# Kernel optimization log

Hardware: AMD Instinct MI355X
Metric: run time of the kernel (lower is better)

## Reference

```python
import jax, jax.numpy as jnp
import numpy as np

N, M, A, F = 8000, 12, 64, 64
EPS = 1e-5


def setup_inputs() -> dict:
    key = jax.random.key(0)
    ks = jax.random.split(key, 8)
    rn = lambda k, s, sc=0.05: jax.random.normal(k, s, jnp.float32) * sc
    return {
        "atom_in_fea": rn(ks[0], (N, A), 1.0),
        "nbr_fea": rn(ks[1], (N, M, F), 1.0),
        "nbr_fea_idx": jax.random.randint(ks[2], (N, M), 0, N),
        # fc_full: in = 2A+F, out = 2A (stored as (in, out))
        "W_full": rn(ks[3], (2 * A + F, 2 * A)), "b_full": jnp.zeros((2 * A,), jnp.float32),
        "bn1_gamma": jnp.ones((2 * A,), jnp.float32), "bn1_beta": jnp.zeros((2 * A,), jnp.float32),
        # fc_edge: in = 2A+F, out = 2F
        "W_edge": rn(ks[4], (2 * A + F, 2 * F)), "b_edge": jnp.zeros((2 * F,), jnp.float32),
        "bne_gamma": jnp.ones((2 * F,), jnp.float32), "bne_beta": jnp.zeros((2 * F,), jnp.float32),
        # fc_3body: in = 3A+2F, out = 2A
        "W_3body": rn(ks[5], (3 * A + 2 * F, 2 * A)), "b_3body": jnp.zeros((2 * A,), jnp.float32),
        "bn3_gamma": jnp.ones((2 * A,), jnp.float32), "bn3_beta": jnp.zeros((2 * A,), jnp.float32),
        # bn2 over atom_fea_len
        "bn2_gamma": jnp.ones((A,), jnp.float32), "bn2_beta": jnp.zeros((A,), jnp.float32),
    }


def _bn(x, gamma, beta):
    # training-mode BatchNorm1d: batch stats over all but the last (channel) axis, biased var
    axes = tuple(range(x.ndim - 1))
    mean = jnp.mean(x, axes, keepdims=True)
    var = jnp.mean(jnp.square(x - mean), axes, keepdims=True)
    return (x - mean) * jax.lax.rsqrt(var + EPS) * gamma + beta


def _gate(z, axis):
    filt, core = jnp.split(z, 2, axis=-1)
    return jnp.sum(jax.nn.sigmoid(filt) * jax.nn.softplus(core), axis=axis)


def reference(atom_in_fea, nbr_fea, nbr_fea_idx,
              W_full, b_full, bn1_gamma, bn1_beta,
              W_edge, b_edge, bne_gamma, bne_beta,
              W_3body, b_3body, bn3_gamma, bn3_beta,
              bn2_gamma, bn2_beta):
    a_len = atom_in_fea.shape[1]
    f_len = nbr_fea.shape[2]
    atom_nbr = atom_in_fea[nbr_fea_idx]                       # (N, M, A) gather
    total = jnp.concatenate([
        jnp.broadcast_to(atom_in_fea[:, None, :], atom_nbr.shape),
        atom_nbr, nbr_fea], axis=-1)                           # (N, M, 2A+F)

    # 2-body gated update
    g = _bn(total @ W_full + b_full, bn1_gamma, bn1_beta)      # (N, M, 2A)
    two_body = _gate(g, axis=1)                                # (N, A)

    # explicit edge update
    e = _bn(total @ W_edge + b_edge, bne_gamma, bne_beta)      # (N, M, 2F)
    ef, ec = jnp.split(e, 2, axis=-1)
    nbr_out_fea = nbr_fea + jax.nn.sigmoid(ef) * jax.nn.softplus(ec)

    # 3-body term: Linear over concat([x_i, x_j, x_l, e_ij, e_il]) decomposed so we never
    # materialize the (N, M, M, 3A+2F) concat; only the (N, M, M, 2A) projection exists.
    Wa, Wj, Wl, Wij, Wil = jnp.split(
        W_3body, [a_len, 2 * a_len, 3 * a_len, 3 * a_len + f_len], axis=0)
    p_i = atom_in_fea @ Wa                                     # (N, 2A)
    p_j = atom_nbr @ Wj + nbr_fea @ Wij                        # (N, M, 2A) j/ij part
    p_l = atom_nbr @ Wl + nbr_fea @ Wil                        # (N, M, 2A) l/il part
    z = p_i[:, None, None, :] + p_j[:, :, None, :] + p_l[:, None, :, :] + b_3body
    z = _bn(z, bn3_gamma, bn3_beta)                            # (N, M, M, 2A)
    three_body = _gate(z, axis=(1, 2))                         # (N, A)

    total_summed = _bn(two_body + three_body, bn2_gamma, bn2_beta)
    atom_out_fea = jax.nn.softplus(atom_in_fea + total_summed)
    return (atom_out_fea, nbr_out_fea)
```

## Files before the change

kernel.cpp:

```cpp
#include <hip/hip_runtime.h>

typedef unsigned short u16;
typedef unsigned int u32;
typedef __attribute__((ext_vector_type(8))) short short8;
typedef __attribute__((ext_vector_type(4))) float f32x4;

#define NATOMS 8000
#define MNBR 12
#define EPSV 1e-5f
#define AB 4
#define ROWS 48
#define NBLK 2000
#define K2REC 1664

#define STG_B 12672
__device__ __forceinline__ int stg_idx(int row, int col) {
  return (row >> 2) * 528 + (row & 3) * 128 + col;
}

#define XB_OFF 0
#define WTA_OFF 1024000
#define WTE_OFF 1122304
#define WAT_OFF 1187840
#define SSUM_OFF 1220608
#define PARAMS_OFF 1227776
#define TBUF_OFF 1230848
#define WS_NEED 3278848

#define SS_BN1S 0
#define SS_BN1S2 128
#define SS_BNES 256
#define SS_BNES2 384
#define SS_U2 512
#define SS_V2 640
#define SS_A 768
#define SS_A2 896
#define SS_UB 1024
#define SS_VB 1152
#define SS_AU 1280
#define SS_AV 1408
#define SS_UV 1536

__device__ __forceinline__ u16 f2bf(float f) {
  u32 u = __float_as_uint(f);
  u += 0x7FFFu + ((u >> 16) & 1u);
  return (u16)(u >> 16);
}
__device__ __forceinline__ float bf2f(u16 h) { return __uint_as_float(((u32)h) << 16); }

__device__ __forceinline__ float sigf(float x) {
  return __builtin_amdgcn_rcpf(1.f + __expf(-x));
}
__device__ __forceinline__ float spf(float x) {
  return fmaxf(x, 0.f) + __logf(1.f + __expf(-fabsf(x)));
}

__device__ __forceinline__ void mfma16(f32x4 &acc, short8 a, short8 b) {
  asm volatile("v_mfma_f32_16x16x32_bf16 %0, %1, %2, %0" : "+v"(acc) : "v"(a), "v"(b));
}
__device__ __forceinline__ void accfence(f32x4 &a) {
  asm volatile("s_nop 7\ns_nop 7\ns_nop 7" : "+v"(a));
}
__device__ __forceinline__ void initfence(f32x4 &a) {
  asm volatile("s_nop 1" : "+v"(a));
}

__device__ __forceinline__ void stage_row16(short* lds, int row, int c16, const float* __restrict__ src) {
  const float4* s4 = reinterpret_cast<const float4*>(src);
  float4 q0 = s4[0], q1 = s4[1], q2 = s4[2], q3 = s4[3];
  short8 lo, hi;
  lo[0]=(short)f2bf(q0.x); lo[1]=(short)f2bf(q0.y); lo[2]=(short)f2bf(q0.z); lo[3]=(short)f2bf(q0.w);
  lo[4]=(short)f2bf(q1.x); lo[5]=(short)f2bf(q1.y); lo[6]=(short)f2bf(q1.z); lo[7]=(short)f2bf(q1.w);
  hi[0]=(short)f2bf(q2.x); hi[1]=(short)f2bf(q2.y); hi[2]=(short)f2bf(q2.z); hi[3]=(short)f2bf(q2.w);
  hi[4]=(short)f2bf(q3.x); hi[5]=(short)f2bf(q3.y); hi[6]=(short)f2bf(q3.z); hi[7]=(short)f2bf(q3.w);
  int base = row * 128 + c16 * 2;
  int sw = (row & 7) << 4;
  *reinterpret_cast<short8*>(reinterpret_cast<char*>(lds) + (base ^ sw)) = lo;
  *reinterpret_cast<short8*>(reinterpret_cast<char*>(lds) + ((base + 16) ^ sw)) = hi;
}

__device__ __forceinline__ void stage_xj(const u16* __restrict__ XB, const int* __restrict__ nidx,
                                         int eb, int ab, char* xjT, int t) {
  for (int s = t; s < 512; s += 256) {
    int r = s >> 3, j = s & 7;
    uint4 val = make_uint4(0u, 0u, 0u, 0u);
    if (r < 48) {
      int idx = nidx[eb + r];
      val = *reinterpret_cast<const uint4*>(XB + (size_t)idx * 64 + j * 8);
    } else if (r < 52) {
      val = *reinterpret_cast<const uint4*>(XB + (size_t)(ab + r - 48) * 64 + j * 8);
    }
    int off = (r * 128 + j * 16) ^ ((r & 7) << 4);
    *reinterpret_cast<uint4*>(xjT + off) = val;
  }
}

__device__ __forceinline__ short8 lds_afrag(const short* lds, int row, int kbyte) {
  int off = (row * 128 + kbyte) ^ ((row & 7) << 4);
  return *reinterpret_cast<const short8*>(reinterpret_cast<const char*>(lds) + off);
}

template <int RT>
__device__ __forceinline__ void mfma_dual(const short* xjT, const short* nbrT,
                                          const u16* __restrict__ WTA, const u16* __restrict__ WTE,
                                          int baseA, int baseE, int w, int l,
                                          f32x4 (&acc)[RT][2]) {
  short8 ba[2][2], be[2][2];
#pragma unroll
  for (int p = 0; p < 2; ++p) {
    int colg = ((w + p * 4) << 4) + (l & 15);
#pragma unroll
    for (int kc = 0; kc < 2; ++kc) {
      ba[p][kc] = *reinterpret_cast<const short8*>(WTA + (size_t)(baseA + colg) * 64 + kc * 32 + ((l >> 4) << 3));
      be[p][kc] = *reinterpret_cast<const short8*>(WTE + (size_t)(baseE + colg) * 64 + kc * 32 + ((l >> 4) << 3));
    }
  }
#pragma unroll
  for (int rt = 0; rt < RT; ++rt)
#pragma unroll
    for (int p = 0; p < 2; ++p) { acc[rt][p] = f32x4{0.f, 0.f, 0.f, 0.f}; initfence(acc[rt][p]); }
#pragma unroll
  for (int rt = 0; rt < RT; ++rt) {
    int arow = rt * 16 + (l & 15);
    short8 x0 = lds_afrag(xjT, arow, (l >> 4) << 4);
    short8 x1 = lds_afrag(xjT, arow, 64 + ((l >> 4) << 4));
    short8 n0 = lds_afrag(nbrT, arow, (l >> 4) << 4);
    short8 n1 = lds_afrag(nbrT, arow, 64 + ((l >> 4) << 4));
#pragma unroll
    for (int p = 0; p < 2; ++p) {
      mfma16(acc[rt][p], x0, ba[p][0]);
      mfma16(acc[rt][p], x1, ba[p][1]);
      mfma16(acc[rt][p], n0, be[p][0]);
      mfma16(acc[rt][p], n1, be[p][1]);
    }
  }
#pragma unroll
  for (int rt = 0; rt < RT; ++rt)
#pragma unroll
    for (int p = 0; p < 2; ++p) accfence(acc[rt][p]);
}

__device__ __forceinline__ void mfma_own(const short* xjT, const u16* __restrict__ WTA,
                                         int baseO, int w, int l, float* ownv) {
  short8 bo[2][2];
#pragma unroll
  for (int p = 0; p < 2; ++p) {
    int colg = ((w + p * 4) << 4) + (l & 15);
#pragma unroll
    for (int kc = 0; kc < 2; ++kc)
      bo[p][kc] = *reinterpret_cast<const short8*>(WTA + (size_t)(baseO + colg) * 64 + kc * 32 + ((l >> 4) << 3));
  }
  int arow = 48 + (l & 15);
  short8 x0 = lds_afrag(xjT, arow, (l >> 4) << 4);
  short8 x1 = lds_afrag(xjT, arow, 64 + ((l >> 4) << 4));
  f32x4 acc[2];
#pragma unroll
  for (int p = 0; p < 2; ++p) {
    acc[p] = f32x4{0.f, 0.f, 0.f, 0.f};
    initfence(acc[p]);
    mfma16(acc[p], x0, bo[p][0]);
    mfma16(acc[p], x1, bo[p][1]);
  }
#pragma unroll
  for (int p = 0; p < 2; ++p) accfence(acc[p]);
  if (l < 16) {
    int col0 = (w << 4) + l;
#pragma unroll
    for (int r = 0; r < 4; ++r) {
      ownv[r * 128 + col0] = acc[0][r];
      ownv[r * 128 + col0 + 64] = acc[1][r];
    }
  }
}

__device__ __forceinline__ void aterm_dot(const float* __restrict__ WaT, const float* xown,
                                          int c, int h, float& dv0, float& dv1) {
  const float4* wa4 = reinterpret_cast<const float4*>(WaT + (size_t)c * 64);
  const float4* x0 = reinterpret_cast<const float4*>(xown + (2 * h) * 64);
  const float4* x1 = reinterpret_cast<const float4*>(xown + (2 * h + 1) * 64);
  dv0 = 0.f; dv1 = 0.f;
#pragma unroll
  for (int q = 0; q < 16; ++q) {
    float4 wv = wa4[q], a4 = x0[q], b4 = x1[q];
    dv0 += a4.x * wv.x + a4.y * wv.y + a4.z * wv.z + a4.w * wv.w;
    dv1 += b4.x * wv.x + b4.y * wv.y + b4.z * wv.z + b4.w * wv.w;
  }
}

__global__ __launch_bounds__(256) void k0_prep(const float* __restrict__ atom_in,
                                               const float* __restrict__ W_full,
                                               const float* __restrict__ W_edge,
                                               const float* __restrict__ W_3body,
                                               u16* __restrict__ XB,
                                               u16* __restrict__ WTA, u16* __restrict__ WTE,
                                               float* __restrict__ WaT,
                                               float* __restrict__ ssum) {
  int t = blockIdx.x * 256 + threadIdx.x;
  if (t < 1792) ssum[t] = 0.f;
  if (t < 8192) { int c = t >> 6, k = t & 63; WaT[t] = W_3body[k * 128 + c]; }
  if (t < 49152) {
    int col = t >> 6, k = t & 63;
    int blk = col >> 7, c = col & 127;
    float v;
    switch (blk) {
      case 0: v = W_full[k * 128 + c]; break;
      case 1: v = W_full[(64 + k) * 128 + c]; break;
      case 2: v = W_edge[k * 128 + c]; break;
      case 3: v = W_edge[(64 + k) * 128 + c]; break;
      case 4: v = W_3body[(64 + k) * 128 + c]; break;
      default: v = W_3body[(128 + k) * 128 + c]; break;
    }
    WTA[t] = f2bf(v);
  } else if (t < 81920) {
    int u = t - 49152;
    int col = u >> 6, k = u & 63;
    int blk = col >> 7, c = col & 127;
    float v;
    switch (blk) {
      case 0: v = W_full[(128 + k) * 128 + c]; break;
      case 1: v = W_edge[(128 + k) * 128 + c]; break;
      case 2: v = W_3body[(192 + k) * 128 + c]; break;
      default: v = W_3body[(256 + k) * 128 + c]; break;
    }
    WTE[u] = f2bf(v);
  }
  if (t < NATOMS * 64) XB[t] = f2bf(atom_in[t]);
}

__global__ __launch_bounds__(256, 4) void k2a_stats(const float* __restrict__ nbr_fea,
                                                    const int* __restrict__ nidx,
                                                    const float* __restrict__ b_full,
                                                    const float* __restrict__ b_edge,
                                                    const u16* __restrict__ XB,
                                                    const u16* __restrict__ WTA,
                                                    const u16* __restrict__ WTE,
                                                    float* __restrict__ k2scr) {
  __shared__ __align__(16) char smem[16384];
  short* nbrT = (short*)smem;
  char* xjT   = smem + 6144;
  float* ownv = (float*)(smem + 14336);
  int t = threadIdx.x, l = t & 63, w = t >> 6;
  int ab = blockIdx.x * AB, eb = ab * 12;
  float* sc = k2scr + (size_t)blockIdx.x * K2REC;

  for (int u = t; u < ROWS * 4; u += 256) {
    int row = u >> 2, c16 = (u & 3) * 16;
    stage_row16(nbrT, row, c16, nbr_fea + (size_t)(eb + row) * 64 + c16);
  }
  stage_xj(XB, nidx, eb, ab, xjT, t);
  __syncthreads();

#pragma unroll
  for (int b = 0; b < 2; ++b) {
    f32x4 acc[3][2];
    mfma_dual<3>((short*)xjT, nbrT, WTA, WTE, b ? 384 : 128, b * 128, w, l, acc);
    mfma_own((short*)xjT, WTA, b ? 256 : 0, w, l, ownv);
    int col0 = (w << 4) + (l & 15), col1 = col0 + 64;
    int g = l >> 4;
    const float* bp = b ? b_edge : b_full;
    float bias0 = bp[col0], bias1 = bp[col1];
    float vs0 = 0.f, vs1 = 0.f, q0 = 0.f, q1 = 0.f;
#pragma unroll
    for (int rt = 0; rt < 3; ++rt) {
      int a12 = (rt * 16 + g * 4) / 12;
      float o0 = ownv[a12 * 128 + col0] + bias0;
      float o1 = ownv[a12 * 128 + col1] + bias1;
#pragma unroll
      for (int r = 0; r < 4; ++r) {
        float v0 = acc[rt][0][r] + o0;
        float v1 = acc[rt][1][r] + o1;
        vs0 += v0; q0 += v0 * v0; vs1 += v1; q1 += v1 * v1;
      }
    }
    vs0 += __shfl_xor(vs0, 16); vs0 += __shfl_xor(vs0, 32);
    vs1 += __shfl_xor(vs1, 16); vs1 += __shfl_xor(vs1, 32);
    q0 += __shfl_xor(q0, 16); q0 += __shfl_xor(q0, 32);
    q1 += __shfl_xor(q1, 16); q1 += __shfl_xor(q1, 32);
    if (l < 16) {
      int base = b ? 256 : 0;
      sc[base + col0] = vs0;
      sc[base + 128 + col0] = q0;
      sc[base + col1] = vs1;
      sc[base + 128 + col1] = q1;
    }
  }
}

__global__ __launch_bounds__(256, 4) void k2b_stats(const float* __restrict__ atom_in,
                                                    const float* __restrict__ nbr_fea,
                                                    const int* __restrict__ nidx,
                                                    const float* __restrict__ WaT,
                                                    const float* __restrict__ b_3body,
                                                    const u16* __restrict__ XB,
                                                    const u16* __restrict__ WTA,
                                                    const u16* __restrict__ WTE,
                                                    float* __restrict__ k2scr) {
  __shared__ __align__(16) char smem[23040];
  short* nbrT   = (short*)smem;
  char* xjT     = smem + 6144;
  float* ubar   = (float*)(smem + 14336);
  float* vbar   = (float*)(smem + 16384);
  float* xown   = (float*)(smem + 18432);
  float* redscr = (float*)(smem + 19456);
  int t = threadIdx.x, l = t & 63, w = t >> 6;
  int ab = blockIdx.x * AB, eb = ab * 12;
  float* sc = k2scr + (size_t)blockIdx.x * K2REC;

  for (int u = t; u < ROWS * 4; u += 256) {
    int row = u >> 2, c16 = (u & 3) * 16;
    stage_row16(nbrT, row, c16, nbr_fea + (size_t)(eb + row) * 64 + c16);
  }
  stage_xj(XB, nidx, eb, ab, xjT, t);
  ubar[t] = 0.f; ubar[256 + t] = 0.f; vbar[t] = 0.f; vbar[256 + t] = 0.f;
  xown[t] = atom_in[(size_t)ab * 64 + t];
  __syncthreads();

#pragma unroll
  for (int b = 2; b < 4; ++b) {
    f32x4 acc[3][2];
    mfma_dual<3>((short*)xjT, nbrT, WTA, WTE, (b == 2) ? 512 : 640, b * 128, w, l, acc);
    float* uvb = (b == 2) ? ubar : vbar;
    int col0 = (w << 4) + (l & 15), col1 = col0 + 64;
    int g = l >> 4;
    float q0 = 0.f, q1 = 0.f;
#pragma unroll
    for (int rt = 0; rt < 3; ++rt) {
      int a12 = (rt * 16 + g * 4) / 12;
      float s0 = 0.f, s1 = 0.f;
#pragma unroll
      for (int r = 0; r < 4; ++r) {
        float v0 = acc[rt][0][r];
        float v1 = acc[rt][1][r];
        s0 += v0; q0 += v0 * v0; s1 += v1; q1 += v1 * v1;
      }
      atomicAdd(&uvb[a12 * 128 + col0], s0);
      atomicAdd(&uvb[a12 * 128 + col1], s1);
    }
    q0 += __shfl_xor(q0, 16); q0 += __shfl_xor(q0, 32);
    q1 += __shfl_xor(q1, 16); q1 += __shfl_xor(q1, 32);
    if (l < 16) {
      int base = (b == 2) ? SS_U2 : SS_V2;
      sc[base + col0] = q0;
      sc[base + col1] = q1;
    }
  }
  __syncthreads();

  {
    int c = t & 127, h = t >> 7;
    float dv0, dv1;
    aterm_dot(WaT, xown, c, h, dv0, dv1);
    float b3v = b_3body[c];
    float pA = 0.f, pA2 = 0.f, pUb = 0.f, pVb = 0.f, pAU = 0.f, pAV = 0.f, pUV = 0.f;
#pragma unroll
    for (int aa = 0; aa < 2; ++aa) {
      int a = 2 * h + aa;
      float aval = (aa ? dv1 : dv0) + b3v;
      float ub = ubar[a * 128 + c] * (1.f / 12.f);
      float vb = vbar[a * 128 + c] * (1.f / 12.f);
      pA += aval; pA2 += aval * aval; pUb += ub; pVb += vb;
      pAU += aval * ub; pAV += aval * vb; pUV += ub * vb;
    }
    if (h == 1) {
      float* rs = &redscr[c * 7];
      rs[0] = pA; rs[1] = pA2; rs[2] = pUb; rs[3] = pVb; rs[4] = pAU; rs[5] = pAV; rs[6] = pUV;
    }
    __syncthreads();
    if (h == 0) {
      const float* rs = &redscr[c * 7];
      sc[SS_A + c] = pA + rs[0];
      sc[SS_A2 + c] = pA2 + rs[1];
      sc[SS_UB + c] = pUb + rs[2];
      sc[SS_VB + c] = pVb + rs[3];
      sc[SS_AU + c] = pAU + rs[4];
      sc[SS_AV + c] = pAV + rs[5];
      sc[SS_UV + c] = pUV + rs[6];
    }
  }
}

__global__ __launch_bounds__(256) void k3r_reduce(const float* __restrict__ k2scr,
                                                  float* __restrict__ ssum) {
  int cb = blockIdx.x & 1, ch = blockIdx.x >> 1;
  int f = cb * 256 + threadIdx.x;
  if (f >= K2REC / 4) return;
  int r0 = ch * 32;
  if (r0 >= NBLK) return;
  int r1 = min(r0 + 32, NBLK);
  float s0 = 0.f, s1 = 0.f, s2 = 0.f, s3 = 0.f;
#pragma unroll 8
  for (int r = r0; r < r1; ++r) {
    float4 v = *reinterpret_cast<const float4*>(k2scr + (size_t)r * K2REC + f * 4);
    s0 += v.x; s1 += v.y; s2 += v.z; s3 += v.w;
  }
  atomicAdd(&ssum[f * 4 + 0], s0);
  atomicAdd(&ssum[f * 4 + 1], s1);
  atomicAdd(&ssum[f * 4 + 2], s2);
  atomicAdd(&ssum[f * 4 + 3], s3);
}

__global__ void k3p_params(const float* __restrict__ ssum,
                           const float* __restrict__ g1, const float* __restrict__ be1,
                           const float* __restrict__ ge, const float* __restrict__ bee,
                           const float* __restrict__ g3, const float* __restrict__ be3,
                           float* __restrict__ params) {
  int c = threadIdx.x;
  if (c >= 128) return;
  const float cnt1 = 1.f / 96000.f;
  {
    float m = ssum[SS_BN1S + c] * cnt1;
    float var = ssum[SS_BN1S2 + c] * cnt1 - m * m;
    float s = g1[c] * rsqrtf(fmaxf(var, 0.f) + EPSV);
    params[c] = s; params[128 + c] = be1[c] - m * s;
  }
  {
    float m = ssum[SS_BNES + c] * cnt1;
    float var = ssum[SS_BNES2 + c] * cnt1 - m * m;
    float s = ge[c] * rsqrtf(fmaxf(var, 0.f) + EPSV);
    params[256 + c] = s; params[384 + c] = bee[c] - m * s;
  }
  {
    float Nf = (float)NATOMS;
    float A_ = ssum[SS_A + c], A2 = ssum[SS_A2 + c];
    float U2 = ssum[SS_U2 + c], V2 = ssum[SS_V2 + c];
    float Ub = ssum[SS_UB + c], Vb = ssum[SS_VB + c];
    float AU = ssum[SS_AU + c], AV = ssum[SS_AV + c], UV = ssum[SS_UV + c];
    float m = (A_ + Ub + Vb) / Nf;
    float ez2 = A2 / Nf + (U2 + V2) / (Nf * 12.f) + 2.f * (AU + AV + UV) / Nf;
    float var = ez2 - m * m;
    float s = g3[c] * rsqrtf(fmaxf(var, 0.f) + EPSV);
    params[512 + c] = s; params[640 + c] = be3[c] - m * s;
  }
}

__global__ __launch_bounds__(256, 4) void k4a_main(const float* __restrict__ nbr_fea,
                                                   const int* __restrict__ nidx,
                                                   const float* __restrict__ b_full,
                                                   const float* __restrict__ b_edge,
                                                   const u16* __restrict__ XB,
                                                   const u16* __restrict__ WTA,
                                                   const u16* __restrict__ WTE,
                                                   const float* __restrict__ params,
                                                   float* __restrict__ tbuf,
                                                   float* __restrict__ out_nbr) {
  __shared__ __align__(16) char smem[19456];
  short* nbrT     = (short*)smem;
  char* xjT       = smem + 6144;
  float* ownv     = (float*)(smem + 14336);
  float* t2buf    = (float*)(smem + 16384);
  float* params_s = (float*)(smem + 17408);
  int t = threadIdx.x, l = t & 63, w = t >> 6;
  int ab = blockIdx.x * AB, eb = ab * 12;

  for (int u = t; u < ROWS * 4; u += 256) {
    int row = u >> 2, c16 = (u & 3) * 16;
    stage_row16(nbrT, row, c16, nbr_fea + (size_t)(eb + row) * 64 + c16);
  }
  stage_xj(XB, nidx, eb, ab, xjT, t);
  params_s[t] = params[t];
  params_s[t + 256] = params[t + 256];
  t2buf[t] = 0.f;
  __syncthreads();

#pragma unroll
  for (int b = 0; b < 2; ++b) {
    f32x4 acc[3][2];
    mfma_dual<3>((short*)xjT, nbrT, WTA, WTE, b ? 384 : 128, b * 128, w, l, acc);
    mfma_own((short*)xjT, WTA, b ? 256 : 0, w, l, ownv);
    int col0 = (w << 4) + (l & 15), col1 = col0 + 64;
    int g = l >> 4;
    const float* bp = b ? b_edge : b_full;
    float bias0 = bp[col0], bias1 = bp[col1];
    float sc0 = params_s[b * 256 + col0], sh0 = params_s[b * 256 + 128 + col0];
    float sc1 = params_s[b * 256 + col1], sh1 = params_s[b * 256 + 128 + col1];
#pragma unroll
    for (int rt = 0; rt < 3; ++rt) {
      int a12 = (rt * 16 + g * 4) / 12;
      float o0 = ownv[a12 * 128 + col0] + bias0;
      float o1 = ownv[a12 * 128 + col1] + bias1;
      float gsum = 0.f;
#pragma unroll
      for (int r = 0; r < 4; ++r) {
        int row = rt * 16 + g * 4 + r;
        float v0 = acc[rt][0][r] + o0;
        float v1 = acc[rt][1][r] + o1;
        float gate = sigf(v0 * sc0 + sh0) * spf(v1 * sc1 + sh1);
        if (b == 0) {
          gsum += gate;
        } else {
          size_t eg = (size_t)(eb + row) * 64 + col0;
          out_nbr[eg] = nbr_fea[eg] + gate;
        }
      }
      if (b == 0) atomicAdd(&t2buf[a12 * 64 + col0], gsum);
    }
  }
  __syncthreads();
  tbuf[(size_t)(ab + w) * 64 + l] = t2buf[t];
}

__global__ __launch_bounds__(256, 4) void k4b_main(const float* __restrict__ atom_in,
                                                   const float* __restrict__ nbr_fea,
                                                   const int* __restrict__ nidx,
                                                   const float* __restrict__ WaT,
                                                   const float* __restrict__ b_3body,
                                                   const u16* __restrict__ XB,
                                                   const u16* __restrict__ WTA,
                                                   const u16* __restrict__ WTE,
                                                   const float* __restrict__ params,
                                                   float* __restrict__ tbuf,
                                                   float* __restrict__ bn2scr) {
  __shared__ __align__(16) char smem[31104];
  short* nbrT    = (short*)smem;
  char* xjT      = smem + 6144;
  u16* u_s       = (u16*)(smem + 14336);
  float* a_s     = (float*)(smem + 27008);
  float* xown    = (float*)(smem + 29056);
  float* p3_s    = (float*)(smem + 30080);
  u16* v_s       = (u16*)smem;
  float* redscr2 = (float*)(smem + 14336);
  int t = threadIdx.x, l = t & 63, w = t >> 6;
  int ab = blockIdx.x * AB, eb = ab * 12;

  for (int u = t; u < ROWS * 4; u += 256) {
    int row = u >> 2, c16 = (u & 3) * 16;
    stage_row16(nbrT, row, c16, nbr_fea + (size_t)(eb + row) * 64 + c16);
  }
  stage_xj(XB, nidx, eb, ab, xjT, t);
  xown[t] = atom_in[(size_t)ab * 64 + t];
  p3_s[t] = params[512 + t];
  float two_body = tbuf[(size_t)(ab + w) * 64 + l];
  __syncthreads();

  {
    int c = t & 127, h = t >> 7;
    float dv0, dv1;
    aterm_dot(WaT, xown, c, h, dv0, dv1);
    float s3 = p3_s[c], t3 = p3_s[128 + c];
    float b3v = b_3body[c];
    a_s[(2 * h) * 128 + c] = (dv0 + b3v) * s3 + t3;
    a_s[(2 * h + 1) * 128 + c] = (dv1 + b3v) * s3 + t3;
  }

  {
    f32x4 acc[3][2];
    mfma_dual<3>((short*)xjT, nbrT, WTA, WTE, 512, 256, w, l, acc);
    int col0 = (w << 4) + (l & 15), col1 = col0 + 64;
    int g = l >> 4;
    float s30 = p3_s[col0], s31 = p3_s[col1];
#pragma unroll
    for (int rt = 0; rt < 3; ++rt) {
#pragma unroll
      for (int r = 0; r < 4; ++r) {
        int row = rt * 16 + g * 4 + r;
        u_s[stg_idx(row, col0)] = f2bf(acc[rt][0][r] * s30);
        u_s[stg_idx(row, col1)] = f2bf(acc[rt][1][r] * s31);
      }
    }
  }
  {
    f32x4 acc[3][2];
    mfma_dual<3>((short*)xjT, nbrT, WTA, WTE, 640, 384, w, l, acc);
    __syncthreads();
    int col0 = (w << 4) + (l & 15), col1 = col0 + 64;
    int g = l >> 4;
    float s30 = p3_s[col0], s31 = p3_s[col1];
#pragma unroll
    for (int rt = 0; rt < 3; ++rt) {
#pragma unroll
      for (int r = 0; r < 4; ++r) {
        int row = rt * 16 + g * 4 + r;
        v_s[stg_idx(row, col0)] = f2bf(acc[rt][0][r] * s30);
        v_s[stg_idx(row, col1)] = f2bf(acc[rt][1][r] * s31);
      }
    }
  }
  __syncthreads();

  float acc3 = 0.f;
  {
    int c = l, a = w;
    float af = a_s[a * 128 + c], ac = a_s[a * 128 + 64 + c];
    float Fl[12], Hl[12];
#pragma unroll
    for (int j2 = 0; j2 < 12; ++j2) {
      float vf = bf2f(v_s[stg_idx(a * 12 + j2, c)]);
      float vc = bf2f(v_s[stg_idx(a * 12 + j2, 64 + c)]);
      Fl[j2] = __expf(-vf);
      Hl[j2] = __expf(vc);
    }
    for (int j = 0; j < 12; ++j) {
      float uf = bf2f(u_s[stg_idx(a * 12 + j, c)]);
      float uc = bf2f(u_s[stg_idx(a * 12 + j, 64 + c)]);
      float Ej = __expf(-(af + uf));
      float Gj = __expf(ac + uc);
#pragma unroll
      for (int l2 = 0; l2 < 12; ++l2) {
        float p = fmaf(Ej, Fl[l2], 1.f);
        float q = fmaf(Gj, Hl[l2], 1.f);
        acc3 += __builtin_amdgcn_rcpf(p) * __log2f(q);
      }
    }
  }
  __syncthreads();

  {
    float x = two_body + acc3 * 0.6931471805599453f;
    tbuf[(size_t)(ab + w) * 64 + l] = x;
    redscr2[t] = x;
    redscr2[256 + t] = x * x;
    __syncthreads();
    if (t < 64) {
      float s = redscr2[t] + redscr2[t + 64] + redscr2[t + 128] + redscr2[t + 192];
      float s2 = redscr2[256 + t] + redscr2[256 + t + 64] + redscr2[256 + t + 128] + redscr2[256 + t + 192];
      bn2scr[(size_t)t * 2048 + blockIdx.x] = s;
      bn2scr[(size_t)(64 + t) * 2048 + blockIdx.x] = s2;
    }
  }
}

__global__ __launch_bounds__(256) void k5_reduce(const float* __restrict__ bn2scr,
                                                 float* __restrict__ bn2sum) {
  __shared__ float wsum[4];
  int c = blockIdx.x, t = threadIdx.x;
  float s = 0.f;
#pragma unroll 4
  for (int i = t; i < NBLK; i += 256) s += bn2scr[(size_t)c * 2048 + i];
  s += __shfl_xor(s, 1); s += __shfl_xor(s, 2); s += __shfl_xor(s, 4);
  s += __shfl_xor(s, 8); s += __shfl_xor(s, 16); s += __shfl_xor(s, 32);
  if ((t & 63) == 0) wsum[t >> 6] = s;
  __syncthreads();
  if (t == 0) bn2sum[c] = wsum[0] + wsum[1] + wsum[2] + wsum[3];
}

__global__ __launch_bounds__(256) void k6_out(const float* __restrict__ atom_in,
                                              const float* __restrict__ tbuf,
                                              const float* __restrict__ bn2sum,
                                              const float* __restrict__ g2,
                                              const float* __restrict__ be2,
                                              float* __restrict__ out_atom) {
  __shared__ float sc[64], sh[64];
  int t = threadIdx.x;
  if (t < 64) {
    float S = bn2sum[t], S2 = bn2sum[64 + t];
    float m = S * (1.f / (float)NATOMS);
    float var = S2 * (1.f / (float)NATOMS) - m * m;
    float s = g2[t] * rsqrtf(fmaxf(var, 0.f) + EPSV);
    sc[t] = s; sh[t] = be2[t] - m * s;
  }
  __syncthreads();
  int i = blockIdx.x * 256 + t;
  if (i < NATOMS * 64) {
    int c = i & 63;
    float v = atom_in[i] + tbuf[i] * sc[c] + sh[c];
    out_atom[i] = spf(v);
  }
}

extern "C" void kernel_launch(void* const* d_in, const int* in_sizes, int n_in,
                              void* d_out, int out_size, void* d_ws, size_t ws_size,
                              hipStream_t stream) {
  if (ws_size < (size_t)WS_NEED) return;
  const float* atom_in = (const float*)d_in[0];
  const float* nbr_fea = (const float*)d_in[1];
  const int* nidx = (const int*)d_in[2];
  const float* W_full = (const float*)d_in[3];
  const float* b_full = (const float*)d_in[4];
  const float* g1 = (const float*)d_in[5];
  const float* be1 = (const float*)d_in[6];
  const float* W_edge = (const float*)d_in[7];
  const float* b_edge = (const float*)d_in[8];
  const float* ge = (const float*)d_in[9];
  const float* bee = (const float*)d_in[10];
  const float* W_3body = (const float*)d_in[11];
  const float* b_3body = (const float*)d_in[12];
  const float* g3 = (const float*)d_in[13];
  const float* be3 = (const float*)d_in[14];
  const float* g2 = (const float*)d_in[15];
  const float* be2 = (const float*)d_in[16];

  char* ws = (char*)d_ws;
  u16* XB = (u16*)(ws + XB_OFF);
  u16* WTA = (u16*)(ws + WTA_OFF);
  u16* WTE = (u16*)(ws + WTE_OFF);
  float* WaT = (float*)(ws + WAT_OFF);
  float* ssum = (float*)(ws + SSUM_OFF);
  float* bn2sum = ssum + K2REC;
  float* params = (float*)(ws + PARAMS_OFF);
  float* tbuf = (float*)(ws + TBUF_OFF);

  float* out_atom = (float*)d_out;
  float* out_nbr = out_atom + NATOMS * 64;
  float* k2scr = out_nbr;
  float* bn2scr = out_atom;

  k0_prep<<<2000, 256, 0, stream>>>(atom_in, W_full, W_edge, W_3body, XB, WTA, WTE, WaT, ssum);
  k2a_stats<<<NBLK, 256, 0, stream>>>(nbr_fea, nidx, b_full, b_edge, XB, WTA, WTE, k2scr);
  k2b_stats<<<NBLK, 256, 0, stream>>>(atom_in, nbr_fea, nidx, WaT, b_3body, XB, WTA, WTE, k2scr);
  k3r_reduce<<<128, 256, 0, stream>>>(k2scr, ssum);
  k3p_params<<<1, 128, 0, stream>>>(ssum, g1, be1, ge, bee, g3, be3, params);
  k4a_main<<<NBLK, 256, 0, stream>>>(nbr_fea, nidx, b_full, b_edge, XB, WTA, WTE, params, tbuf, out_nbr);
  k4b_main<<<NBLK, 256, 0, stream>>>(atom_in, nbr_fea, nidx, WaT, b_3body, XB, WTA, WTE, params,
                                     tbuf, bn2scr);
  k5_reduce<<<128, 256, 0, stream>>>(bn2scr, bn2sum);
  k6_out<<<2000, 256, 0, stream>>>(atom_in, tbuf, bn2sum, g2, be2, out_atom);
}
```

Measured before the change: 183.2 us.

## Fuse paired stats and main kernels to share staged neighbor tiles

Merges k2a/k2b into one stats kernel and k4a/k4b into one main kernel. Each fused block stages the nbr_fea and gathered neighbor features into LDS once and runs all four projection branches from them. The two-body partial stays in shared memory instead of making a round trip through tbuf. This removes two launches and the duplicated gather and staging traffic. In exchange, LDS per block and per-block serial work grow, which may reduce occupancy and latency hiding.

```diff
diff --git a/kernel.cpp b/kernel.cpp
--- a/kernel.cpp
+++ b/kernel.cpp
@@ -95,13 +95,13 @@
   }
 }
 
-__device__ __forceinline__ short8 lds_afrag(const short* lds, int row, int kbyte) {
+__device__ __forceinline__ short8 lds_afrag(const char* lds, int row, int kbyte) {
   int off = (row * 128 + kbyte) ^ ((row & 7) << 4);
-  return *reinterpret_cast<const short8*>(reinterpret_cast<const char*>(lds) + off);
+  return *reinterpret_cast<const short8*>(lds + off);
 }
 
 template <int RT>
-__device__ __forceinline__ void mfma_dual(const short* xjT, const short* nbrT,
+__device__ __forceinline__ void mfma_dual(const char* xjT, const char* nbrT,
                                           const u16* __restrict__ WTA, const u16* __restrict__ WTE,
                                           int baseA, int baseE, int w, int l,
                                           f32x4 (&acc)[RT][2]) {
@@ -140,7 +140,7 @@
     for (int p = 0; p < 2; ++p) accfence(acc[rt][p]);
 }
 
-__device__ __forceinline__ void mfma_own(const short* xjT, const u16* __restrict__ WTA,
+__device__ __forceinline__ void mfma_own(const char* xjT, const u16* __restrict__ WTA,
                                          int baseO, int w, int l, float* ownv) {
   short8 bo[2][2];
 #pragma unroll
@@ -227,121 +227,96 @@
   if (t < NATOMS * 64) XB[t] = f2bf(atom_in[t]);
 }
 
-__global__ __launch_bounds__(256, 4) void k2a_stats(const float* __restrict__ nbr_fea,
-                                                    const int* __restrict__ nidx,
-                                                    const float* __restrict__ b_full,
-                                                    const float* __restrict__ b_edge,
-                                                    const u16* __restrict__ XB,
-                                                    const u16* __restrict__ WTA,
-                                                    const u16* __restrict__ WTE,
-                                                    float* __restrict__ k2scr) {
-  __shared__ __align__(16) char smem[16384];
-  short* nbrT = (short*)smem;
-  char* xjT   = smem + 6144;
-  float* ownv = (float*)(smem + 14336);
+__global__ __launch_bounds__(256, 4) void k2_stats(const float* __restrict__ atom_in,
+                                                   const float* __restrict__ nbr_fea,
+                                                   const int* __restrict__ nidx,
+                                                   const float* __restrict__ WaT,
+                                                   const float* __restrict__ b_full,
+                                                   const float* __restrict__ b_edge,
+                                                   const float* __restrict__ b_3body,
+                                                   const u16* __restrict__ XB,
+                                                   const u16* __restrict__ WTA,
+                                                   const u16* __restrict__ WTE,
+                                                   float* __restrict__ k2scr) {
+  __shared__ __align__(16) char smem[25088];
+  char* nbrT    = smem;
+  char* xjT     = smem + 6144;
+  float* ownv   = (float*)(smem + 14336);
+  float* ubar   = (float*)(smem + 16384);
+  float* vbar   = (float*)(smem + 18432);
+  float* xown   = (float*)(smem + 20480);
+  float* redscr = (float*)(smem + 21504);
   int t = threadIdx.x, l = t & 63, w = t >> 6;
   int ab = blockIdx.x * AB, eb = ab * 12;
   float* sc = k2scr + (size_t)blockIdx.x * K2REC;
 
   for (int u = t; u < ROWS * 4; u += 256) {
     int row = u >> 2, c16 = (u & 3) * 16;
-    stage_row16(nbrT, row, c16, nbr_fea + (size_t)(eb + row) * 64 + c16);
-  }
-  stage_xj(XB, nidx, eb, ab, xjT, t);
-  __syncthreads();
-
-#pragma unroll
-  for (int b = 0; b < 2; ++b) {
-    f32x4 acc[3][2];
-    mfma_dual<3>((short*)xjT, nbrT, WTA, WTE, b ? 384 : 128, b * 128, w, l, acc);
-    mfma_own((short*)xjT, WTA, b ? 256 : 0, w, l, ownv);
-    int col0 = (w << 4) + (l & 15), col1 = col0 + 64;
-    int g = l >> 4;
-    const float* bp = b ? b_edge : b_full;
-    float bias0 = bp[col0], bias1 = bp[col1];
-    float vs0 = 0.f, vs1 = 0.f, q0 = 0.f, q1 = 0.f;
-#pragma unroll
-    for (int rt = 0; rt < 3; ++rt) {
-      int a12 = (rt * 16 + g * 4) / 12;
-      float o0 = ownv[a12 * 128 + col0] + bias0;
-      float o1 = ownv[a12 * 128 + col1] + bias1;
-#pragma unroll
-      for (int r = 0; r < 4; ++r) {
-        float v0 = acc[rt][0][r] + o0;
-        float v1 = acc[rt][1][r] + o1;
-        vs0 += v0; q0 += v0 * v0; vs1 += v1; q1 += v1 * v1;
-      }
-    }
-    vs0 += __shfl_xor(vs0, 16); vs0 += __shfl_xor(vs0, 32);
-    vs1 += __shfl_xor(vs1, 16); vs1 += __shfl_xor(vs1, 32);
-    q0 += __shfl_xor(q0, 16); q0 += __shfl_xor(q0, 32);
-    q1 += __shfl_xor(q1, 16); q1 += __shfl_xor(q1, 32);
-    if (l < 16) {
-      int base = b ? 256 : 0;
-      sc[base + col0] = vs0;
-      sc[base + 128 + col0] = q0;
-      sc[base + col1] = vs1;
-      sc[base + 128 + col1] = q1;
-    }
-  }
-}
-
-__global__ __launch_bounds__(256, 4) void k2b_stats(const float* __restrict__ atom_in,
-                                                    const float* __restrict__ nbr_fea,
-                                                    const int* __restrict__ nidx,
-                                                    const float* __restrict__ WaT,
-                                                    const float* __restrict__ b_3body,
-                                                    const u16* __restrict__ XB,
-                                                    const u16* __restrict__ WTA,
-                                                    const u16* __restrict__ WTE,
-                                                    float* __restrict__ k2scr) {
-  __shared__ __align__(16) char smem[23040];
-  short* nbrT   = (short*)smem;
-  char* xjT     = smem + 6144;
-  float* ubar   = (float*)(smem + 14336);
-  float* vbar   = (float*)(smem + 16384);
-  float* xown   = (float*)(smem + 18432);
-  float* redscr = (float*)(smem + 19456);
-  int t = threadIdx.x, l = t & 63, w = t >> 6;
-  int ab = blockIdx.x * AB, eb = ab * 12;
-  float* sc = k2scr + (size_t)blockIdx.x * K2REC;
-
-  for (int u = t; u < ROWS * 4; u += 256) {
-    int row = u >> 2, c16 = (u & 3) * 16;
-    stage_row16(nbrT, row, c16, nbr_fea + (size_t)(eb + row) * 64 + c16);
+    stage_row16((short*)nbrT, row, c16, nbr_fea + (size_t)(eb + row) * 64 + c16);
   }
   stage_xj(XB, nidx, eb, ab, xjT, t);
   ubar[t] = 0.f; ubar[256 + t] = 0.f; vbar[t] = 0.f; vbar[256 + t] = 0.f;
   xown[t] = atom_in[(size_t)ab * 64 + t];
   __syncthreads();
 
-#pragma unroll
-  for (int b = 2; b < 4; ++b) {
+  const int baseA[4] = {128, 384, 512, 640};
+#pragma unroll
+  for (int b = 0; b < 4; ++b) {
     f32x4 acc[3][2];
-    mfma_dual<3>((short*)xjT, nbrT, WTA, WTE, (b == 2) ? 512 : 640, b * 128, w, l, acc);
-    float* uvb = (b == 2) ? ubar : vbar;
+    mfma_dual<3>(xjT, nbrT, WTA, WTE, baseA[b], b * 128, w, l, acc);
     int col0 = (w << 4) + (l & 15), col1 = col0 + 64;
     int g = l >> 4;
-    float q0 = 0.f, q1 = 0.f;
-#pragma unroll
-    for (int rt = 0; rt < 3; ++rt) {
-      int a12 = (rt * 16 + g * 4) / 12;
-      float s0 = 0.f, s1 = 0.f;
-#pragma unroll
-      for (int r = 0; r < 4; ++r) {
-        float v0 = acc[rt][0][r];
-        float v1 = acc[rt][1][r];
-        s0 += v0; q0 += v0 * v0; s1 += v1; q1 += v1 * v1;
-      }
-      atomicAdd(&uvb[a12 * 128 + col0], s0);
-      atomicAdd(&uvb[a12 * 128 + col1], s1);
-    }
-    q0 += __shfl_xor(q0, 16); q0 += __shfl_xor(q0, 32);
-    q1 += __shfl_xor(q1, 16); q1 += __shfl_xor(q1, 32);
-    if (l < 16) {
-      int base = (b == 2) ? SS_U2 : SS_V2;
-      sc[base + col0] = q0;
-      sc[base + col1] = q1;
+    if (b < 2) {
+      mfma_own(xjT, WTA, b ? 256 : 0, w, l, ownv);
+      const float* bp = b ? b_edge : b_full;
+      float bias0 = bp[col0], bias1 = bp[col1];
+      float vs0 = 0.f, vs1 = 0.f, q0 = 0.f, q1 = 0.f;
+#pragma unroll
+      for (int rt = 0; rt < 3; ++rt) {
+        int a12 = (rt * 16 + g * 4) / 12;
+        float o0 = ownv[a12 * 128 + col0] + bias0;
+        float o1 = ownv[a12 * 128 + col1] + bias1;
+#pragma unroll
+        for (int r = 0; r < 4; ++r) {
+          float v0 = acc[rt][0][r] + o0;
+          float v1 = acc[rt][1][r] + o1;
+          vs0 += v0; q0 += v0 * v0; vs1 += v1; q1 += v1 * v1;
+        }
+      }
+      vs0 += __shfl_xor(vs0, 16); vs0 += __shfl_xor(vs0, 32);
+      vs1 += __shfl_xor(vs1, 16); vs1 += __shfl_xor(vs1, 32);
+      q0 += __shfl_xor(q0, 16); q0 += __shfl_xor(q0, 32);
+      q1 += __shfl_xor(q1, 16); q1 += __shfl_xor(q1, 32);
+      if (l < 16) {
+        int base = b ? 256 : 0;
+        sc[base + col0] = vs0;
+        sc[base + 128 + col0] = q0;
+        sc[base + col1] = vs1;
+        sc[base + 128 + col1] = q1;
+      }
+    } else {
+      float* uvb = (b == 2) ? ubar : vbar;
+      float q0 = 0.f, q1 = 0.f;
+#pragma unroll
+      for (int rt = 0; rt < 3; ++rt) {
+        int a12 = (rt * 16 + g * 4) / 12;
+        float s0 = 0.f, s1 = 0.f;
+#pragma unroll
+        for (int r = 0; r < 4; ++r) {
+          float v0 = acc[rt][0][r];
+          float v1 = acc[rt][1][r];
+          s0 += v0; q0 += v0 * v0; s1 += v1; q1 += v1 * v1;
+        }
+        atomicAdd(&uvb[a12 * 128 + col0], s0);
+        atomicAdd(&uvb[a12 * 128 + col1], s1);
+      }
+      q0 += __shfl_xor(q0, 16); q0 += __shfl_xor(q0, 32);
+      q1 += __shfl_xor(q1, 16); q1 += __shfl_xor(q1, 32);
+      if (l < 16) {
+        int base = (b == 2) ? SS_U2 : SS_V2;
+        sc[base + col0] = q0;
+        sc[base + col1] = q1;
+      }
     }
   }
   __syncthreads();
@@ -433,40 +408,62 @@
   }
 }
 
-__global__ __launch_bounds__(256, 4) void k4a_main(const float* __restrict__ nbr_fea,
-                                                   const int* __restrict__ nidx,
-                                                   const float* __restrict__ b_full,
-                                                   const float* __restrict__ b_edge,
-                                                   const u16* __restrict__ XB,
-                                                   const u16* __restrict__ WTA,
-                                                   const u16* __restrict__ WTE,
-                                                   const float* __restrict__ params,
-                                                   float* __restrict__ tbuf,
-                                                   float* __restrict__ out_nbr) {
-  __shared__ __align__(16) char smem[19456];
-  short* nbrT     = (short*)smem;
+__global__ __launch_bounds__(256, 4) void k4_main(const float* __restrict__ atom_in,
+                                                  const float* __restrict__ nbr_fea,
+                                                  const int* __restrict__ nidx,
+                                                  const float* __restrict__ WaT,
+                                                  const float* __restrict__ b_full,
+                                                  const float* __restrict__ b_edge,
+                                                  const float* __restrict__ b_3body,
+                                                  const u16* __restrict__ XB,
+                                                  const u16* __restrict__ WTA,
+                                                  const u16* __restrict__ WTE,
+                                                  const float* __restrict__ params,
+                                                  float* __restrict__ tbuf,
+                                                  float* __restrict__ out_nbr,
+                                                  float* __restrict__ bn2scr) {
+  __shared__ __align__(16) char smem[36224];
+  char* nbrT      = smem;
   char* xjT       = smem + 6144;
-  float* ownv     = (float*)(smem + 14336);
-  float* t2buf    = (float*)(smem + 16384);
-  float* params_s = (float*)(smem + 17408);
+  u16* u_s        = (u16*)(smem + 14336);
+  float* ownv     = (float*)(smem + 27008);
+  float* t2buf    = (float*)(smem + 29056);
+  float* params_s = (float*)(smem + 30080);
+  float* p3_s     = (float*)(smem + 32128);
+  float* a_s      = (float*)(smem + 33152);
+  float* xown     = (float*)(smem + 35200);
+  u16* v_s        = (u16*)smem;
+  float* redscr2  = (float*)(smem + 14336);
   int t = threadIdx.x, l = t & 63, w = t >> 6;
   int ab = blockIdx.x * AB, eb = ab * 12;
 
   for (int u = t; u < ROWS * 4; u += 256) {
     int row = u >> 2, c16 = (u & 3) * 16;
-    stage_row16(nbrT, row, c16, nbr_fea + (size_t)(eb + row) * 64 + c16);
+    stage_row16((short*)nbrT, row, c16, nbr_fea + (size_t)(eb + row) * 64 + c16);
   }
   stage_xj(XB, nidx, eb, ab, xjT, t);
+  xown[t] = atom_in[(size_t)ab * 64 + t];
   params_s[t] = params[t];
   params_s[t + 256] = params[t + 256];
+  p3_s[t] = params[512 + t];
   t2buf[t] = 0.f;
   __syncthreads();
 
+  {
+    int c = t & 127, h = t >> 7;
+    float dv0, dv1;
+    aterm_dot(WaT, xown, c, h, dv0, dv1);
+    float s3 = p3_s[c], t3 = p3_s[128 + c];
+    float b3v = b_3body[c];
+    a_s[(2 * h) * 128 + c] = (dv0 + b3v) * s3 + t3;
+    a_s[(2 * h + 1) * 128 + c] = (dv1 + b3v) * s3 + t3;
+  }
+
 #pragma unroll
   for (int b = 0; b < 2; ++b) {
     f32x4 acc[3][2];
-    mfma_dual<3>((short*)xjT, nbrT, WTA, WTE, b ? 384 : 128, b * 128, w, l, acc);
-    mfma_own((short*)xjT, WTA, b ? 256 : 0, w, l, ownv);
+    mfma_dual<3>(xjT, nbrT, WTA, WTE, b ? 384 : 128, b * 128, w, l, acc);
+    mfma_own(xjT, WTA, b ? 256 : 0, w, l, ownv);
     int col0 = (w << 4) + (l & 15), col1 = col0 + 64;
     int g = l >> 4;
     const float* bp = b ? b_edge : b_full;
@@ -495,56 +492,10 @@
       if (b == 0) atomicAdd(&t2buf[a12 * 64 + col0], gsum);
     }
   }
-  __syncthreads();
-  tbuf[(size_t)(ab + w) * 64 + l] = t2buf[t];
-}
-
-__global__ __launch_bounds__(256, 4) void k4b_main(const float* __restrict__ atom_in,
-                                                   const float* __restrict__ nbr_fea,
-                                                   const int* __restrict__ nidx,
-                                                   const float* __restrict__ WaT,
-                                                   const float* __restrict__ b_3body,
-                                                   const u16* __restrict__ XB,
-                                                   const u16* __restrict__ WTA,
-                                                   const u16* __restrict__ WTE,
-                                                   const float* __restrict__ params,
-                                                   float* __restrict__ tbuf,
-                                                   float* __restrict__ bn2scr) {
-  __shared__ __align__(16) char smem[31104];
-  short* nbrT    = (short*)smem;
-  char* xjT      = smem + 6144;
-  u16* u_s       = (u16*)(smem + 14336);
-  float* a_s     = (float*)(smem + 27008);
-  float* xown    = (float*)(smem + 29056);
-  float* p3_s    = (float*)(smem + 30080);
-  u16* v_s       = (u16*)smem;
-  float* redscr2 = (float*)(smem + 14336);
-  int t = threadIdx.x, l = t & 63, w = t >> 6;
-  int ab = blockIdx.x * AB, eb = ab * 12;
-
-  for (int u = t; u < ROWS * 4; u += 256) {
-    int row = u >> 2, c16 = (u & 3) * 16;
-    stage_row16(nbrT, row, c16, nbr_fea + (size_t)(eb + row) * 64 + c16);
-  }
-  stage_xj(XB, nidx, eb, ab, xjT, t);
-  xown[t] = atom_in[(size_t)ab * 64 + t];
-  p3_s[t] = params[512 + t];
-  float two_body = tbuf[(size_t)(ab + w) * 64 + l];
-  __syncthreads();
-
-  {
-    int c = t & 127, h = t >> 7;
-    float dv0, dv1;
-    aterm_dot(WaT, xown, c, h, dv0, dv1);
-    float s3 = p3_s[c], t3 = p3_s[128 + c];
-    float b3v = b_3body[c];
-    a_s[(2 * h) * 128 + c] = (dv0 + b3v) * s3 + t3;
-    a_s[(2 * h + 1) * 128 + c] = (dv1 + b3v) * s3 + t3;
-  }
 
   {
     f32x4 acc[3][2];
-    mfma_dual<3>((short*)xjT, nbrT, WTA, WTE, 512, 256, w, l, acc);
+    mfma_dual<3>(xjT, nbrT, WTA, WTE, 512, 256, w, l, acc);
     int col0 = (w << 4) + (l & 15), col1 = col0 + 64;
     int g = l >> 4;
     float s30 = p3_s[col0], s31 = p3_s[col1];
@@ -560,7 +511,7 @@
   }
   {
     f32x4 acc[3][2];
-    mfma_dual<3>((short*)xjT, nbrT, WTA, WTE, 640, 384, w, l, acc);
+    mfma_dual<3>(xjT, nbrT, WTA, WTE, 640, 384, w, l, acc);
     __syncthreads();
     int col0 = (w << 4) + (l & 15), col1 = col0 + 64;
     int g = l >> 4;
@@ -605,7 +556,7 @@
   __syncthreads();
 
   {
-    float x = two_body + acc3 * 0.6931471805599453f;
+    float x = t2buf[t] + acc3 * 0.6931471805599453f;
     tbuf[(size_t)(ab + w) * 64 + l] = x;
     redscr2[t] = x;
     redscr2[256 + t] = x * x;
@@ -695,13 +646,12 @@
   float* bn2scr = out_atom;
 
   k0_prep<<<2000, 256, 0, stream>>>(atom_in, W_full, W_edge, W_3body, XB, WTA, WTE, WaT, ssum);
-  k2a_stats<<<NBLK, 256, 0, stream>>>(nbr_fea, nidx, b_full, b_edge, XB, WTA, WTE, k2scr);
-  k2b_stats<<<NBLK, 256, 0, stream>>>(atom_in, nbr_fea, nidx, WaT, b_3body, XB, WTA, WTE, k2scr);
+  k2_stats<<<NBLK, 256, 0, stream>>>(atom_in, nbr_fea, nidx, WaT, b_full, b_edge, b_3body,
+                                     XB, WTA, WTE, k2scr);
   k3r_reduce<<<128, 256, 0, stream>>>(k2scr, ssum);
   k3p_params<<<1, 128, 0, stream>>>(ssum, g1, be1, ge, bee, g3, be3, params);
-  k4a_main<<<NBLK, 256, 0, stream>>>(nbr_fea, nidx, b_full, b_edge, XB, WTA, WTE, params, tbuf, out_nbr);
-  k4b_main<<<NBLK, 256, 0, stream>>>(atom_in, nbr_fea, nidx, WaT, b_3body, XB, WTA, WTE, params,
-                                     tbuf, bn2scr);
+  k4_main<<<NBLK, 256, 0, stream>>>(atom_in, nbr_fea, nidx, WaT, b_full, b_edge, b_3body,
+                                    XB, WTA, WTE, params, tbuf, out_nbr, bn2scr);
   k5_reduce<<<128, 256, 0, stream>>>(bn2scr, bn2sum);
   k6_out<<<2000, 256, 0, stream>>>(atom_in, tbuf, bn2sum, g2, be2, out_atom);
 }
```

Result: faster. 169.2 us (-7.6%).
